# Kernel optimization log

Hardware: AMD Instinct MI355X
Metric: run time of the kernel (lower is better)

## Reference

```python
import jax, jax.numpy as jnp
import numpy as np
import math

B, S, D, H_HEADS, K_SPAN = 2, 2048, 64, 12, 512  # batch, seq, head dim, heads, pos_ebd_size


def setup_inputs() -> dict:
    key = jax.random.key(0)
    ks = jax.random.split(key, 12)
    init = lambda k, shp: (jax.random.normal(k, shp, dtype=jnp.float32) * 0.02)
    H = jax.random.normal(ks[0], (B, S, D), dtype=jnp.float32)
    pos_embeddings = jax.random.normal(ks[1], (2 * K_SPAN, D), dtype=jnp.float32)
    # classic DeBERTa relative positions: i - j (2-D, as required by the torch code path)
    idx = jnp.arange(S)
    relative_pos = (idx[:, None] - idx[None, :]).astype(jnp.int64)
    OH = H_HEADS * D
    return {
        "H": H,
        "pos_embeddings": pos_embeddings,
        "relative_pos": relative_pos,
        "Wq": init(ks[2], (OH, D)), "bq": jnp.zeros((OH,), jnp.float32),
        "Wk": init(ks[3], (OH, D)), "bk": jnp.zeros((OH,), jnp.float32),
        "Wv": init(ks[4], (OH, D)), "bv": jnp.zeros((OH,), jnp.float32),
        "Wpq": init(ks[5], (OH, D)), "bpq": jnp.zeros((OH,), jnp.float32),
        "Wpk": init(ks[6], (OH, D)), "bpk": jnp.zeros((OH,), jnp.float32),
    }


def _heads(x):
    # [..., S, h*d] -> [..., h, S, d]
    b, s, _ = x.shape
    return x.reshape(b, s, H_HEADS, D).transpose(0, 2, 1, 3)


def reference(H, pos_embeddings, relative_pos, Wq, bq, Wk, bk, Wv, bv, Wpq, bpq, Wpk, bpk):
    proj = lambda x, W, b: x @ W.T + b
    q = _heads(proj(H, Wq, bq))  # [B,h,S,d]
    k = _heads(proj(H, Wk, bk))
    v = _heads(proj(H, Wv, bv))

    # content-to-content scores
    scores = jnp.einsum('bhqd,bhkd->bhqk', q, k)  # [B,h,S,S]

    # relative position projections over the full 2K span
    pk = proj(pos_embeddings, Wpk, bpk).reshape(2 * K_SPAN, H_HEADS, D).transpose(1, 0, 2)  # [h,2K,d]
    pq = proj(pos_embeddings, Wpq, bpq).reshape(2 * K_SPAN, H_HEADS, D).transpose(1, 0, 2)

    rel = relative_pos.astype(jnp.int32)
    # content-to-position: gather over 2K axis with clamped (i-j)+K
    c2p = jnp.einsum('bhqd,hrd->bhqr', q, pk)  # [B,h,S,2K]
    c2p_pos = jnp.clip(rel + K_SPAN, 0, 2 * K_SPAN - 1)  # [S,S]
    c2p_idx = jnp.broadcast_to(c2p_pos[None, None], (B, H_HEADS, S, S))
    c2p_att = jnp.take_along_axis(c2p, c2p_idx, axis=-1)  # [B,h,S,S]

    # position-to-content: gather over 2K axis with clamped -(i-j)+K, then transpose
    p2c = jnp.einsum('bhkd,hrd->bhkr', k, pq)  # [B,h,S,2K]
    p2c_pos = jnp.clip(-rel + K_SPAN, 0, 2 * K_SPAN - 1)
    p2c_idx = jnp.broadcast_to(p2c_pos[None, None], (B, H_HEADS, S, S))
    p2c_att = jnp.take_along_axis(p2c, p2c_idx, axis=-1).swapaxes(-1, -2)  # [B,h,S,S]

    scores = (scores + c2p_att + p2c_att) / math.sqrt(D * 3)
    probs = jax.nn.softmax(scores, axis=-1)
    ctx = jnp.einsum('bhqk,bhkd->bhqd', probs, v)  # [B,h,S,d]
    return ctx.transpose(0, 2, 1, 3).reshape(B, S, H_HEADS * D)
```

## Files before the change

kernel.cpp:

```cpp
#include <hip/hip_runtime.h>
#include <math.h>


#define S_LEN 2048
#define NH    12
#define TWOK  1024
#define QSZ   3145728
#define PSZ   786432

typedef __bf16 bf16x8 __attribute__((ext_vector_type(8)));
typedef unsigned short u16x8 __attribute__((ext_vector_type(8)));
typedef float f32x4  __attribute__((ext_vector_type(4)));
typedef float f32x16 __attribute__((ext_vector_type(16)));
typedef unsigned int u32x2 __attribute__((ext_vector_type(2)));
typedef unsigned int u32x4 __attribute__((ext_vector_type(4)));

__device__ __forceinline__ unsigned short f2bf(float f) {
  return __builtin_bit_cast(unsigned short, (__bf16)f);
}
__device__ __forceinline__ unsigned pk2bf(float a, float b) {
  return ((unsigned)__builtin_bit_cast(unsigned short, (__bf16)b) << 16)
       | (unsigned)__builtin_bit_cast(unsigned short, (__bf16)a);
}
__device__ __forceinline__ float bf2f(unsigned short h) {
  return __builtin_bit_cast(float, ((unsigned)h) << 16);
}
__device__ __forceinline__ bf16x8 ld_bf8(const unsigned short* p) {
  return __builtin_bit_cast(bf16x8, *(const u16x8*)p);
}

__global__ __launch_bounds__(256) void prep_kernel(
    const float* __restrict__ Hx, const float* __restrict__ pos,
    const float* __restrict__ Wq, const float* __restrict__ Wk,
    const float* __restrict__ Wv, const float* __restrict__ Wpk,
    const float* __restrict__ Wpq,
    const float* __restrict__ bq, const float* __restrict__ bk,
    const float* __restrict__ bv, const float* __restrict__ bpk,
    const float* __restrict__ bpq,
    unsigned short* __restrict__ whi, unsigned short* __restrict__ wlo,
    unsigned short* __restrict__ wall, float* __restrict__ ball) {
  int idx = blockIdx.x * 256 + threadIdx.x;
  if (idx < 327680) {
    float v = (idx < 262144) ? Hx[idx] : pos[idx - 262144];
    __bf16 hi = (__bf16)v;
    float lo = v - (float)hi;
    whi[idx] = __builtin_bit_cast(unsigned short, hi);
    wlo[idx] = f2bf(lo);
  } else if (idx < 573440) {
    int k = idx - 327680;
    int mat = k / 49152, off = k - mat * 49152;
    const float* W = mat==0?Wq: mat==1?Wk: mat==2?Wv: mat==3?Wpk:Wpq;
    wall[k] = f2bf(W[off]);
  } else if (idx < 577280) {
    int k = idx - 573440;
    int mat = k / 768, off = k - mat * 768;
    const float* B = mat==0?bq: mat==1?bk: mat==2?bv: mat==3?bpk:bpq;
    ball[k] = B[off];
  }
}

__global__ __launch_bounds__(256) void proj_gemm(
    const unsigned short* __restrict__ whi, const unsigned short* __restrict__ wlo,
    const unsigned short* __restrict__ wall, const float* __restrict__ ball,
    unsigned short* __restrict__ ws) {
  unsigned short* qg  = ws;
  unsigned short* kg  = ws + QSZ;
  unsigned short* vtg = ws + 2 * QSZ;
  unsigned short* pkg = ws + 3 * QSZ;
  unsigned short* pqg = ws + 3 * QSZ + PSZ;

  int bid = blockIdx.x;
  int rbase, obase, wrow, isA;
  if (bid < 2304) { rbase = (bid / 36) * 64;        obase = (bid % 36) * 64; wrow = obase;        isA = 1; }
  else { int b2 = bid - 2304; rbase = 4096 + (b2 / 24) * 64; obase = (b2 % 24) * 64; wrow = 2304 + obase; isA = 0; }

  int tid = threadIdx.x, w = tid >> 6, l = tid & 63, lg = l >> 4, lr = l & 15;
  int xrow = rbase + w * 16 + lr;

  bf16x8 ah[2], al[2];
  #pragma unroll
  for (int ks = 0; ks < 2; ++ks) {
    ah[ks] = ld_bf8(whi + xrow * 64 + ks * 32 + 8 * lg);
    al[ks] = ld_bf8(wlo + xrow * 64 + ks * 32 + 8 * lg);
  }

  int mat = obase / 768;
  int h = ((obase % 768) >> 6);

  #pragma unroll
  for (int jb = 0; jb < 4; ++jb) {
    f32x4 acc = {0.f, 0.f, 0.f, 0.f};
    #pragma unroll
    for (int ks = 0; ks < 2; ++ks) {
      bf16x8 bfrag = ld_bf8(wall + (wrow + jb * 16 + lr) * 64 + ks * 32 + 8 * lg);
      acc = __builtin_amdgcn_mfma_f32_16x16x32_bf16(ah[ks], bfrag, acc, 0, 0, 0);
      acc = __builtin_amdgcn_mfma_f32_16x16x32_bf16(al[ks], bfrag, acc, 0, 0, 0);
    }
    float bias = ball[wrow + jb * 16 + lr];
    int d = jb * 16 + lr;
    #pragma unroll
    for (int r = 0; r < 4; ++r) {
      int orow = rbase + w * 16 + 4 * lg + r;
      unsigned short val = f2bf(acc[r] + bias);
      if (isA) {
        int bb = orow >> 11, i = orow & 2047, bh = bb * NH + h;
        if (mat == 0)      qg[(bh * S_LEN + i) * 64 + d] = val;
        else if (mat == 1) kg[(bh * S_LEN + i) * 64 + d] = val;
        else               vtg[(bh * 64 + d) * S_LEN + i] = val;
      } else {
        int prow = orow - 4096;
        if (mat == 0) pkg[(h * TWOK + prow) * 64 + d] = val;
        else          pqg[(h * TWOK + prow) * 64 + d] = val;
      }
    }
  }
}

__global__ __launch_bounds__(128, 2) void attn_kernel(
    const unsigned short* __restrict__ ws, float* __restrict__ out) {
  const unsigned short* qg  = ws;
  const unsigned short* kg  = ws + QSZ;
  const unsigned short* vtg = ws + 2 * QSZ;
  const unsigned short* pkg = ws + 3 * QSZ;
  const unsigned short* pqg = ws + 3 * QSZ + PSZ;

  __shared__ __align__(16) unsigned short tblC[2 * 32 * 128];
  __shared__ __align__(16) unsigned short tblP[64 * 128];

  const int bid = blockIdx.x;
  const int bh = bid >> 5, itile = bid & 31;
  const int b = bh / NH, h = bh - b * NH;
  const int tid = threadIdx.x;
  const int w = tid >> 6, l = tid & 63;
  const int iL = l & 31, h5 = l >> 5;

  const unsigned short* qb  = qg  + bh * (S_LEN * 64);
  const unsigned short* kb  = kg  + bh * (S_LEN * 64);
  const unsigned short* vb  = vtg + bh * (64 * S_LEN);
  const unsigned short* pkb = pkg + h * (TWOK * 64);
  const unsigned short* pqb = pqg + h * (TWOK * 64);

  const float CS = 1.4426950408889634f / sqrtf(192.0f);

  const int ig = itile * 64 + w * 32 + iL;
  bf16x8 qf[4];
  #pragma unroll
  for (int kc = 0; kc < 4; ++kc)
    qf[kc] = ld_bf8(qb + ig * 64 + kc * 16 + 8 * h5);

  f32x16 ctx0 = 0.f, ctx1 = 0.f;
  float m_ = -1e30f, l_ = 0.f;

  char* tC = (char*)tblC;
  char* tP = (char*)tblP;
  char* cbase = tC + (w * 32 + iL) * 256;
  const int cxor = (iL & 15) << 4;
  const int prow = w * 32 + iL;
  char* pbase = tP + prow * 256;
  const int pxor = (prow & 15) << 4;

  for (int jt = 0; jt < 32; ++jt) {
    const int j0 = jt * 64;
    int R0 = itile * 64 - j0 + 512;
    int relmin = R0 - 63; relmin = relmin < 0 ? 0 : (relmin > 1023 ? 1023 : relmin);
    int relmax = R0 + 63; relmax = relmax < 0 ? 0 : (relmax > 1023 ? 1023 : relmax);
    int bstart = relmin > 896 ? 896 : relmin;
    int nb_lo = (relmin - bstart) >> 5, nb_hi = (relmax - bstart) >> 5;

    bf16x8 kf0[4], kf1[4];
    #pragma unroll
    for (int kc = 0; kc < 4; ++kc) {
      kf0[kc] = ld_bf8(kb + (j0 + iL) * 64 + kc * 16 + 8 * h5);
      kf1[kc] = ld_bf8(kb + (j0 + 32 + iL) * 64 + kc * 16 + 8 * h5);
    }
    f32x16 s0 = 0.f, s1 = 0.f;
    #pragma unroll
    for (int kc = 0; kc < 4; ++kc) {
      s0 = __builtin_amdgcn_mfma_f32_32x32x16_bf16(kf0[kc], qf[kc], s0, 0, 0, 0);
      s1 = __builtin_amdgcn_mfma_f32_32x32x16_bf16(kf1[kc], qf[kc], s1, 0, 0, 0);
    }
    bf16x8 kp[4];
    #pragma unroll
    for (int kc = 0; kc < 4; ++kc) kp[kc] = w ? kf1[kc] : kf0[kc];

    __syncthreads();

    for (int nb = nb_lo; nb <= nb_hi; ++nb) {
      const int rrow = bstart + nb * 32 + iL;
      f32x16 ac = 0.f, ap = 0.f;
      #pragma unroll
      for (int kc = 0; kc < 4; ++kc) {
        bf16x8 fk = ld_bf8(pkb + rrow * 64 + kc * 16 + 8 * h5);
        bf16x8 fq = ld_bf8(pqb + rrow * 64 + kc * 16 + 8 * h5);
        ac = __builtin_amdgcn_mfma_f32_32x32x16_bf16(fk, qf[kc], ac, 0, 0, 0);
        ap = __builtin_amdgcn_mfma_f32_32x32x16_bf16(fq, kp[kc], ap, 0, 0, 0);
      }
      #pragma unroll
      for (int q4 = 0; q4 < 4; ++q4) {
        int relb = 32 * nb + 8 * q4 + 4 * h5;
        u32x2 vc; vc[0] = pk2bf(ac[4*q4+0], ac[4*q4+1]); vc[1] = pk2bf(ac[4*q4+2], ac[4*q4+3]);
        *(u32x2*)(cbase + ((relb * 2) ^ cxor)) = vc;
        u32x2 vp; vp[0] = pk2bf(ap[4*q4+0], ap[4*q4+1]); vp[1] = pk2bf(ap[4*q4+2], ap[4*q4+3]);
        *(u32x2*)(pbase + ((relb * 2) ^ pxor)) = vp;
      }
    }
    __syncthreads();

    const int D0 = ig + 512 - j0;
    #pragma unroll
    for (int r = 0; r < 16; ++r) {
      const int j32 = (r & 3) + 8 * (r >> 2) + 4 * h5;
      {
        int rel = D0 - j32; rel = rel < 0 ? 0 : (rel > 1023 ? 1023 : rel);
        int rb = rel - bstart;
        float c2 = bf2f(*(const unsigned short*)(cbase + ((rb * 2) ^ cxor)));
        float p2 = bf2f(*(const unsigned short*)(tP + j32 * 256 + ((rb * 2) ^ ((j32 & 15) << 4))));
        s0[r] = (s0[r] + c2 + p2) * CS;
      }
      {
        int jl = 32 + j32;
        int rel = D0 - jl; rel = rel < 0 ? 0 : (rel > 1023 ? 1023 : rel);
        int rb = rel - bstart;
        float c2 = bf2f(*(const unsigned short*)(cbase + ((rb * 2) ^ cxor)));
        float p2 = bf2f(*(const unsigned short*)(tP + jl * 256 + ((rb * 2) ^ ((jl & 15) << 4))));
        s1[r] = (s1[r] + c2 + p2) * CS;
      }
    }

    float vmax = s0[0];
    #pragma unroll
    for (int r = 1; r < 16; ++r) vmax = fmaxf(vmax, s0[r]);
    #pragma unroll
    for (int r = 0; r < 16; ++r) vmax = fmaxf(vmax, s1[r]);
    vmax = fmaxf(vmax, __shfl_xor(vmax, 32));
    float mx = fmaxf(m_, vmax);
    float fs = __builtin_amdgcn_exp2f(m_ - mx);
    m_ = mx;
    float sum = 0.f;
    #pragma unroll
    for (int r = 0; r < 16; ++r) { s0[r] = __builtin_amdgcn_exp2f(s0[r] - mx); sum += s0[r]; }
    #pragma unroll
    for (int r = 0; r < 16; ++r) { s1[r] = __builtin_amdgcn_exp2f(s1[r] - mx); sum += s1[r]; }
    sum += __shfl_xor(sum, 32);
    l_ = l_ * fs + sum;
    ctx0 *= fs; ctx1 *= fs;

    bf16x8 pf[4];
    #pragma unroll
    for (int kc = 0; kc < 4; ++kc) {
      const int c = kc & 1;
      const f32x16& sj = (kc >> 1) ? s1 : s0;
      unsigned X0 = pk2bf(sj[8*c+0], sj[8*c+1]);
      unsigned X1 = pk2bf(sj[8*c+2], sj[8*c+3]);
      unsigned Y0 = pk2bf(sj[8*c+4], sj[8*c+5]);
      unsigned Y1 = pk2bf(sj[8*c+6], sj[8*c+7]);
      unsigned sx0 = (unsigned)__shfl_xor((int)X0, 32);
      unsigned sx1 = (unsigned)__shfl_xor((int)X1, 32);
      unsigned sy0 = (unsigned)__shfl_xor((int)Y0, 32);
      unsigned sy1 = (unsigned)__shfl_xor((int)Y1, 32);
      u32x4 f;
      f[0] = h5 ? sy0 : X0;
      f[1] = h5 ? sy1 : X1;
      f[2] = h5 ? Y0 : sx0;
      f[3] = h5 ? Y1 : sx1;
      pf[kc] = __builtin_bit_cast(bf16x8, f);
    }

    #pragma unroll
    for (int kc = 0; kc < 4; ++kc) {
      bf16x8 v0 = ld_bf8(vb + (iL) * S_LEN + j0 + kc * 16 + 8 * h5);
      bf16x8 v1 = ld_bf8(vb + (32 + iL) * S_LEN + j0 + kc * 16 + 8 * h5);
      ctx0 = __builtin_amdgcn_mfma_f32_32x32x16_bf16(v0, pf[kc], ctx0, 0, 0, 0);
      ctx1 = __builtin_amdgcn_mfma_f32_32x32x16_bf16(v1, pf[kc], ctx1, 0, 0, 0);
    }
  }

  float inv = 1.0f / l_;
  float* ob = out + (b * S_LEN + ig) * 768 + h * 64;
  #pragma unroll
  for (int q4 = 0; q4 < 4; ++q4) {
    float4 o0 = {ctx0[4*q4+0]*inv, ctx0[4*q4+1]*inv, ctx0[4*q4+2]*inv, ctx0[4*q4+3]*inv};
    *(float4*)(ob + 8 * q4 + 4 * h5) = o0;
    float4 o1 = {ctx1[4*q4+0]*inv, ctx1[4*q4+1]*inv, ctx1[4*q4+2]*inv, ctx1[4*q4+3]*inv};
    *(float4*)(ob + 32 + 8 * q4 + 4 * h5) = o1;
  }
}

extern "C" void kernel_launch(void* const* d_in, const int* in_sizes, int n_in,
                              void* d_out, int out_size, void* d_ws, size_t ws_size,
                              hipStream_t stream) {
  (void)in_sizes; (void)n_in; (void)out_size; (void)ws_size;
  const float* Hx  = (const float*)d_in[0];
  const float* pos = (const float*)d_in[1];
  const float* Wq  = (const float*)d_in[3];  const float* bq  = (const float*)d_in[4];
  const float* Wk  = (const float*)d_in[5];  const float* bk  = (const float*)d_in[6];
  const float* Wv  = (const float*)d_in[7];  const float* bv  = (const float*)d_in[8];
  const float* Wpq = (const float*)d_in[9];  const float* bpq = (const float*)d_in[10];
  const float* Wpk = (const float*)d_in[11]; const float* bpk = (const float*)d_in[12];
  unsigned short* ws = (unsigned short*)d_ws;

  unsigned short* scratch = (unsigned short*)d_out;
  unsigned short* whi  = scratch;
  unsigned short* wlo  = scratch + 327680;
  unsigned short* wall = scratch + 655360;
  float*          ball = (float*)(scratch + 901120);

  prep_kernel<<<2255, 256, 0, stream>>>(Hx, pos, Wq, Wk, Wv, Wpk, Wpq,
                                        bq, bk, bv, bpk, bpq, whi, wlo, wall, ball);
  proj_gemm<<<2688, 256, 0, stream>>>(whi, wlo, wall, ball, ws);
  attn_kernel<<<768, 128, 0, stream>>>(ws, (float*)d_out);
}
```

Before: 349.2 us.

## Precompute clamped-edge position dots and skip relative-position MFMAs for saturated tiles

Adds a small kernel that computes q·pk[0], q·pk[1023], k·pq[0], k·pq[1023] for every row. When a tile's relative index is fully clamped, the attention kernel takes these scalars and broadcasts them with shuffles instead of running the position MFMAs and LDS tables. Interior tiles get per-wave P tables and compute p2c MFMAs only for the 32-row blocks each half needs. The two block-wide __syncthreads are dropped in favour of a local lgkmcnt wait, and the context rescale is skipped when the max did not change. The cost is an extra kernel launch, more workspace, and more branching and registers.

New measurement: 345.5 us. No clear change (-1.1%).

```diff
diff --git a/kernel.cpp b/kernel.cpp
--- a/kernel.cpp
+++ b/kernel.cpp
@@ -7,6 +7,7 @@
 #define TWOK  1024
 #define QSZ   3145728
 #define PSZ   786432
+#define POSF  11010048
 
 typedef __bf16 bf16x8 __attribute__((ext_vector_type(8)));
 typedef unsigned short u16x8 __attribute__((ext_vector_type(8)));
@@ -116,6 +117,34 @@
   }
 }
 
+__global__ __launch_bounds__(256) void pos_dots(
+    const unsigned short* __restrict__ ws, float* __restrict__ c2p0,
+    float* __restrict__ c2p1023, float* __restrict__ p2c0,
+    float* __restrict__ p2c1023) {
+  int t = blockIdx.x * 256 + threadIdx.x;
+  int isK = t >= 49152;
+  int row = isK ? t - 49152 : t;
+  int h = (row >> 11) % NH;
+  const unsigned short* src = ws + (isK ? QSZ : 0) + row * 64;
+  const unsigned short* pA = ws + 3 * QSZ + (isK ? PSZ : 0) + (h * TWOK) * 64;
+  const unsigned short* pB = pA + 1023 * 64;
+  float a0 = 0.f, a1 = 0.f;
+  #pragma unroll
+  for (int c = 0; c < 8; ++c) {
+    u16x8 xv = *(const u16x8*)(src + c * 8);
+    u16x8 av = *(const u16x8*)(pA + c * 8);
+    u16x8 bv = *(const u16x8*)(pB + c * 8);
+    #pragma unroll
+    for (int e = 0; e < 8; ++e) {
+      float x = bf2f(xv[e]);
+      a0 += x * bf2f(av[e]);
+      a1 += x * bf2f(bv[e]);
+    }
+  }
+  if (isK) { p2c0[row] = a0; p2c1023[row] = a1; }
+  else     { c2p0[row] = a0; c2p1023[row] = a1; }
+}
+
 __global__ __launch_bounds__(128, 2) void attn_kernel(
     const unsigned short* __restrict__ ws, float* __restrict__ out) {
   const unsigned short* qg  = ws;
@@ -123,9 +152,13 @@
   const unsigned short* vtg = ws + 2 * QSZ;
   const unsigned short* pkg = ws + 3 * QSZ;
   const unsigned short* pqg = ws + 3 * QSZ + PSZ;
+  const float* c2p0g    = (const float*)(ws + POSF);
+  const float* c2p1023g = c2p0g + 49152;
+  const float* p2c0g    = c2p0g + 98304;
+  const float* p2c1023g = c2p0g + 147456;
 
   __shared__ __align__(16) unsigned short tblC[2 * 32 * 128];
-  __shared__ __align__(16) unsigned short tblP[64 * 128];
+  __shared__ __align__(16) unsigned short tblP[2 * 64 * 128];
 
   const int bid = blockIdx.x;
   const int bh = bid >> 5, itile = bid & 31;
@@ -133,6 +166,8 @@
   const int tid = threadIdx.x;
   const int w = tid >> 6, l = tid & 63;
   const int iL = l & 31, h5 = l >> 5;
+  const int i0w = itile * 64 + w * 32;
+  const int ig = i0w + iL;
 
   const unsigned short* qb  = qg  + bh * (S_LEN * 64);
   const unsigned short* kb  = kg  + bh * (S_LEN * 64);
@@ -142,30 +177,27 @@
 
   const float CS = 1.4426950408889634f / sqrtf(192.0f);
 
-  const int ig = itile * 64 + w * 32 + iL;
   bf16x8 qf[4];
   #pragma unroll
   for (int kc = 0; kc < 4; ++kc)
     qf[kc] = ld_bf8(qb + ig * 64 + kc * 16 + 8 * h5);
 
+  const float c2pLO = c2p0g[bh * S_LEN + ig];
+  const float c2pHI = c2p1023g[bh * S_LEN + ig];
+
   f32x16 ctx0 = 0.f, ctx1 = 0.f;
   float m_ = -1e30f, l_ = 0.f;
 
-  char* tC = (char*)tblC;
-  char* tP = (char*)tblP;
-  char* cbase = tC + (w * 32 + iL) * 256;
+  char* cbase = (char*)tblC + w * 8192 + iL * 256;
+  char* tPw   = (char*)tblP + w * 16384;
+  char* pb0   = tPw + iL * 256;
+  char* pb1   = tPw + (32 + iL) * 256;
   const int cxor = (iL & 15) << 4;
-  const int prow = w * 32 + iL;
-  char* pbase = tP + prow * 256;
-  const int pxor = (prow & 15) << 4;
 
   for (int jt = 0; jt < 32; ++jt) {
     const int j0 = jt * 64;
-    int R0 = itile * 64 - j0 + 512;
-    int relmin = R0 - 63; relmin = relmin < 0 ? 0 : (relmin > 1023 ? 1023 : relmin);
-    int relmax = R0 + 63; relmax = relmax < 0 ? 0 : (relmax > 1023 ? 1023 : relmax);
-    int bstart = relmin > 896 ? 896 : relmin;
-    int nb_lo = (relmin - bstart) >> 5, nb_hi = (relmax - bstart) >> 5;
+    const int rlo = 512 + i0w - j0 - 63;
+    const int rhi = rlo + 94;
 
     bf16x8 kf0[4], kf1[4];
     #pragma unroll
@@ -179,51 +211,102 @@
       s0 = __builtin_amdgcn_mfma_f32_32x32x16_bf16(kf0[kc], qf[kc], s0, 0, 0, 0);
       s1 = __builtin_amdgcn_mfma_f32_32x32x16_bf16(kf1[kc], qf[kc], s1, 0, 0, 0);
     }
-    bf16x8 kp[4];
-    #pragma unroll
-    for (int kc = 0; kc < 4; ++kc) kp[kc] = w ? kf1[kc] : kf0[kc];
-
-    __syncthreads();
-
-    for (int nb = nb_lo; nb <= nb_hi; ++nb) {
-      const int rrow = bstart + nb * 32 + iL;
-      f32x16 ac = 0.f, ap = 0.f;
+
+    if (rlo >= 1023) {
+      float pa = p2c1023g[bh * S_LEN + j0 + iL];
+      float pb = p2c1023g[bh * S_LEN + j0 + 32 + iL];
       #pragma unroll
-      for (int kc = 0; kc < 4; ++kc) {
-        bf16x8 fk = ld_bf8(pkb + rrow * 64 + kc * 16 + 8 * h5);
-        bf16x8 fq = ld_bf8(pqb + rrow * 64 + kc * 16 + 8 * h5);
-        ac = __builtin_amdgcn_mfma_f32_32x32x16_bf16(fk, qf[kc], ac, 0, 0, 0);
-        ap = __builtin_amdgcn_mfma_f32_32x32x16_bf16(fq, kp[kc], ap, 0, 0, 0);
+      for (int r = 0; r < 16; ++r) {
+        const int j32 = (r & 3) + 8 * (r >> 2) + 4 * h5;
+        s0[r] = (s0[r] + c2pHI + __shfl(pa, j32)) * CS;
+        s1[r] = (s1[r] + c2pHI + __shfl(pb, j32)) * CS;
       }
+    } else if (rhi <= 0) {
+      float pa = p2c0g[bh * S_LEN + j0 + iL];
+      float pb = p2c0g[bh * S_LEN + j0 + 32 + iL];
       #pragma unroll
-      for (int q4 = 0; q4 < 4; ++q4) {
-        int relb = 32 * nb + 8 * q4 + 4 * h5;
-        u32x2 vc; vc[0] = pk2bf(ac[4*q4+0], ac[4*q4+1]); vc[1] = pk2bf(ac[4*q4+2], ac[4*q4+3]);
-        *(u32x2*)(cbase + ((relb * 2) ^ cxor)) = vc;
-        u32x2 vp; vp[0] = pk2bf(ap[4*q4+0], ap[4*q4+1]); vp[1] = pk2bf(ap[4*q4+2], ap[4*q4+3]);
-        *(u32x2*)(pbase + ((relb * 2) ^ pxor)) = vp;
+      for (int r = 0; r < 16; ++r) {
+        const int j32 = (r & 3) + 8 * (r >> 2) + 4 * h5;
+        s0[r] = (s0[r] + c2pLO + __shfl(pa, j32)) * CS;
+        s1[r] = (s1[r] + c2pLO + __shfl(pb, j32)) * CS;
       }
-    }
-    __syncthreads();
-
-    const int D0 = ig + 512 - j0;
-    #pragma unroll
-    for (int r = 0; r < 16; ++r) {
-      const int j32 = (r & 3) + 8 * (r >> 2) + 4 * h5;
-      {
-        int rel = D0 - j32; rel = rel < 0 ? 0 : (rel > 1023 ? 1023 : rel);
-        int rb = rel - bstart;
-        float c2 = bf2f(*(const unsigned short*)(cbase + ((rb * 2) ^ cxor)));
-        float p2 = bf2f(*(const unsigned short*)(tP + j32 * 256 + ((rb * 2) ^ ((j32 & 15) << 4))));
-        s0[r] = (s0[r] + c2 + p2) * CS;
+    } else {
+      const int rminc = rlo < 0 ? 0 : rlo;
+      const int rmaxc = rhi > 1023 ? 1023 : rhi;
+      const int bstart = rminc > 928 ? 928 : rminc;
+      const int nbh = (rmaxc - bstart) >> 5;
+      const int interior = (rlo >= 0) & (rhi <= 1023);
+      int c_lo = (rminc - bstart) >> 5;
+      int p0_lo, p1_hi;
+      if (interior) {
+        p0_lo = (rlo + 32 - bstart) >> 5;
+        p1_hi = (rhi - 32 - bstart) >> 5;
+      } else { p0_lo = c_lo; p1_hi = nbh; }
+
+      for (int nb = c_lo; nb <= nbh; ++nb) {
+        const int rrow = bstart + nb * 32 + iL;
+        const int doP0 = nb >= p0_lo, doP1 = nb <= p1_hi;
+        f32x16 ac = 0.f, a0 = 0.f, a1 = 0.f;
+        #pragma unroll
+        for (int kc = 0; kc < 4; ++kc) {
+          bf16x8 fk = ld_bf8(pkb + rrow * 64 + kc * 16 + 8 * h5);
+          ac = __builtin_amdgcn_mfma_f32_32x32x16_bf16(fk, qf[kc], ac, 0, 0, 0);
+        }
+        if (doP0 | doP1) {
+          #pragma unroll
+          for (int kc = 0; kc < 4; ++kc) {
+            bf16x8 fq = ld_bf8(pqb + rrow * 64 + kc * 16 + 8 * h5);
+            if (doP0) a0 = __builtin_amdgcn_mfma_f32_32x32x16_bf16(fq, kf0[kc], a0, 0, 0, 0);
+            if (doP1) a1 = __builtin_amdgcn_mfma_f32_32x32x16_bf16(fq, kf1[kc], a1, 0, 0, 0);
+          }
+        }
+        #pragma unroll
+        for (int q4 = 0; q4 < 4; ++q4) {
+          const int off = ((nb * 32 + 8 * q4 + 4 * h5) * 2) ^ cxor;
+          u32x2 vc; vc[0] = pk2bf(ac[4*q4+0], ac[4*q4+1]); vc[1] = pk2bf(ac[4*q4+2], ac[4*q4+3]);
+          *(u32x2*)(cbase + off) = vc;
+          if (doP0) {
+            u32x2 v0; v0[0] = pk2bf(a0[4*q4+0], a0[4*q4+1]); v0[1] = pk2bf(a0[4*q4+2], a0[4*q4+3]);
+            *(u32x2*)(pb0 + off) = v0;
+          }
+          if (doP1) {
+            u32x2 v1; v1[0] = pk2bf(a1[4*q4+0], a1[4*q4+1]); v1[1] = pk2bf(a1[4*q4+2], a1[4*q4+3]);
+            *(u32x2*)(pb1 + off) = v1;
+          }
+        }
       }
-      {
-        int jl = 32 + j32;
-        int rel = D0 - jl; rel = rel < 0 ? 0 : (rel > 1023 ? 1023 : rel);
-        int rb = rel - bstart;
-        float c2 = bf2f(*(const unsigned short*)(cbase + ((rb * 2) ^ cxor)));
-        float p2 = bf2f(*(const unsigned short*)(tP + jl * 256 + ((rb * 2) ^ ((jl & 15) << 4))));
-        s1[r] = (s1[r] + c2 + p2) * CS;
+      asm volatile("s_waitcnt lgkmcnt(0)" ::: "memory");
+
+      const int D0 = ig + 512 - j0;
+      if (interior) {
+        const int t0 = (D0 - bstart) * 2;
+        #pragma unroll
+        for (int r = 0; r < 16; ++r) {
+          const int j32 = (r & 3) + 8 * (r >> 2) + 4 * h5;
+          const int pxr = (j32 & 15) << 4;
+          const int o0 = t0 - 2 * j32, o1 = o0 - 64;
+          float c0v = bf2f(*(const unsigned short*)(cbase + (o0 ^ cxor)));
+          float p0v = bf2f(*(const unsigned short*)(tPw + j32 * 256 + (o0 ^ pxr)));
+          float c1v = bf2f(*(const unsigned short*)(cbase + (o1 ^ cxor)));
+          float p1v = bf2f(*(const unsigned short*)(tPw + (32 + j32) * 256 + (o1 ^ pxr)));
+          s0[r] = (s0[r] + c0v + p0v) * CS;
+          s1[r] = (s1[r] + c1v + p1v) * CS;
+        }
+      } else {
+        #pragma unroll
+        for (int r = 0; r < 16; ++r) {
+          const int j32 = (r & 3) + 8 * (r >> 2) + 4 * h5;
+          const int pxr = (j32 & 15) << 4;
+          int rel0 = D0 - j32;       rel0 = rel0 < 0 ? 0 : (rel0 > 1023 ? 1023 : rel0);
+          int rel1 = D0 - 32 - j32;  rel1 = rel1 < 0 ? 0 : (rel1 > 1023 ? 1023 : rel1);
+          const int o0 = (rel0 - bstart) * 2, o1 = (rel1 - bstart) * 2;
+          float c0v = bf2f(*(const unsigned short*)(cbase + (o0 ^ cxor)));
+          float p0v = bf2f(*(const unsigned short*)(tPw + j32 * 256 + (o0 ^ pxr)));
+          float c1v = bf2f(*(const unsigned short*)(cbase + (o1 ^ cxor)));
+          float p1v = bf2f(*(const unsigned short*)(tPw + (32 + j32) * 256 + (o1 ^ pxr)));
+          s0[r] = (s0[r] + c0v + p0v) * CS;
+          s1[r] = (s1[r] + c1v + p1v) * CS;
+        }
       }
     }
 
@@ -243,7 +326,7 @@
     for (int r = 0; r < 16; ++r) { s1[r] = __builtin_amdgcn_exp2f(s1[r] - mx); sum += s1[r]; }
     sum += __shfl_xor(sum, 32);
     l_ = l_ * fs + sum;
-    ctx0 *= fs; ctx1 *= fs;
+    if (!__all(fs == 1.0f)) { ctx0 *= fs; ctx1 *= fs; }
 
     bf16x8 pf[4];
     #pragma unroll
@@ -305,8 +388,14 @@
   unsigned short* wall = scratch + 655360;
   float*          ball = (float*)(scratch + 901120);
 
+  float* c2p0g    = (float*)(ws + POSF);
+  float* c2p1023g = c2p0g + 49152;
+  float* p2c0g    = c2p0g + 98304;
+  float* p2c1023g = c2p0g + 147456;
+
   prep_kernel<<<2255, 256, 0, stream>>>(Hx, pos, Wq, Wk, Wv, Wpk, Wpq,
                                         bq, bk, bv, bpk, bpq, whi, wlo, wall, ball);
   proj_gemm<<<2688, 256, 0, stream>>>(whi, wlo, wall, ball, ws);
+  pos_dots<<<384, 256, 0, stream>>>(ws, c2p0g, c2p1023g, p2c0g, p2c1023g);
   attn_kernel<<<768, 128, 0, stream>>>(ws, (float*)d_out);
 }
```
